# Optimization experiments

Hardware: AMD Instinct MI355X
Metric: run time of the kernel (lower is better)

## Reference

```python
import jax, jax.numpy as jnp
import numpy as np

B, T, R, E, H = 64, 512, 256, 512, 1024

def setup_inputs() -> dict:
    key = jax.random.key(0)
    ks = jax.random.split(key, 7)
    s = lambda d: 1.0 / np.sqrt(d)
    return {
        "x": jax.random.normal(ks[0], (B, T, R), jnp.float32),
        "W_emb": jax.random.normal(ks[1], (E, R), jnp.float32) * s(R),
        "b_emb": jax.random.normal(ks[2], (E,), jnp.float32) * s(R),
        "W_ih": jax.random.normal(ks[3], (4 * H, E), jnp.float32) * s(H),
        "W_hh": jax.random.normal(ks[4], (4 * H, H), jnp.float32) * s(H),
        "b_ih": jax.random.normal(ks[5], (4 * H,), jnp.float32) * s(H),
        "b_hh": jax.random.normal(ks[6], (4 * H,), jnp.float32) * s(H),
    }

def reference(x, W_emb, b_emb, W_ih, W_hh, b_ih, b_hh):
    # Per-timestep Linear embedding, batched over time (same math as the loop)
    xe = jnp.einsum('btr,er->bte', x, W_emb) + b_emb            # [B,T,E]
    # Input contribution to all gates, precomputed for every step
    gx = jnp.einsum('bte,ge->btg', xe, W_ih) + (b_ih + b_hh)    # [B,T,4H]

    def step(carry, gx_t):
        h, c = carry
        gates = gx_t + h @ W_hh.T                               # [B,4H]
        i, f, g, o = jnp.split(gates, 4, axis=-1)
        i = jax.nn.sigmoid(i)
        f = jax.nn.sigmoid(f)
        g = jnp.tanh(g)
        o = jax.nn.sigmoid(o)
        c_new = f * c + i * g
        h_new = o * jnp.tanh(c_new)
        return (h_new, c_new), h_new

    h0 = jnp.zeros((x.shape[0], H), x.dtype)
    c0 = jnp.zeros((x.shape[0], H), x.dtype)
    (h_t, c_t), ys = jax.lax.scan(step, (h0, c0), jnp.swapaxes(gx, 0, 1))
    outputs = jnp.swapaxes(ys, 0, 1)                            # [B,T,H]
    return outputs, h_t, c_t
```

## Files before the change

### kernel.cpp

```cpp
#include <hip/hip_runtime.h>
#include <stdint.h>

typedef __attribute__((ext_vector_type(8))) short short8;
typedef __attribute__((ext_vector_type(4))) float f32x4;
typedef __attribute__((ext_vector_type(4))) unsigned short ushort4v;
typedef unsigned long long u64;

__device__ inline unsigned short f2bf(float x) {
  union { float f; unsigned u; } v; v.f = x;
  unsigned r = (v.u + 0x7FFFu + ((v.u >> 16) & 1u)) >> 16;
  return (unsigned short)r;
}
__device__ inline float bf2f(unsigned short b) {
  union { unsigned u; float f; } v; v.u = ((unsigned)b) << 16;
  return v.f;
}
__device__ inline float fsig(float x) { return 1.f / (1.f + __expf(-x)); }

__device__ inline void gload_lds16(const void* g, void* l) {
  __builtin_amdgcn_global_load_lds(
      (const __attribute__((address_space(1))) unsigned int*)g,
      (__attribute__((address_space(3))) unsigned int*)l, 16, 0, 0);
}

__global__ void k_convert(const float* __restrict__ src, unsigned short* __restrict__ dst, int n4) {
  int i = blockIdx.x * blockDim.x + threadIdx.x;
  if (i < n4) {
    f32x4 v = *(const f32x4*)(src + (size_t)i * 4);
    ushort4v r;
    r.x = f2bf(v.x); r.y = f2bf(v.y); r.z = f2bf(v.z); r.w = f2bf(v.w);
    *(ushort4v*)(dst + (size_t)i * 4) = r;
  }
}

__global__ void k_bias(const float* __restrict__ a, const float* __restrict__ b,
                       float* __restrict__ o, int n) {
  int i = blockIdx.x * blockDim.x + threadIdx.x;
  if (i < n) o[i] = a[i] + b[i];
}

__global__ void k_init(unsigned short* __restrict__ h0, unsigned short* __restrict__ flags) {
  int i = blockIdx.x * blockDim.x + threadIdx.x;
  h0[i] = 0;
  if (i < 256) flags[i] = 0;
}

template <int MODE>
__global__ __launch_bounds__(256) void k_gemm_bt(
    const unsigned short* __restrict__ A,
    const unsigned short* __restrict__ Bm,
    const float* __restrict__ bias,
    unsigned short* __restrict__ C,
    int M, int N, int K) {
  __shared__ unsigned short As[128 * 32];
  __shared__ unsigned short Bs[128 * 32];
  const int tid = threadIdx.x;
  const int m0 = blockIdx.y * 128, n0 = blockIdx.x * 128;
  const int lane = tid & 63, w = tid >> 6;
  const int wm = (w >> 1) * 64, wn = (w & 1) * 64;

  f32x4 acc[4][4] = {};

  const int ar0 = tid >> 2;
  const int ak = (tid & 3) * 8;
  const unsigned short* Ag0 = A + (size_t)(m0 + ar0) * K + ak;
  const unsigned short* Ag1 = A + (size_t)(m0 + 64 + ar0) * K + ak;
  const unsigned short* Bg0 = Bm + (size_t)(n0 + ar0) * K + ak;
  const unsigned short* Bg1 = Bm + (size_t)(n0 + 64 + ar0) * K + ak;
  unsigned short* Al = As + tid * 8;
  unsigned short* Bl = Bs + tid * 8;

  const int lr = lane & 15, lk = (lane >> 4) * 8;

  for (int k0 = 0; k0 < K; k0 += 32) {
    gload_lds16(Ag0 + k0, Al);
    gload_lds16(Ag1 + k0, Al + 2048);
    gload_lds16(Bg0 + k0, Bl);
    gload_lds16(Bg1 + k0, Bl + 2048);
    __syncthreads();
    short8 a[4], b[4];
#pragma unroll
    for (int i = 0; i < 4; i++) a[i] = *(const short8*)&As[(wm + i * 16 + lr) * 32 + lk];
#pragma unroll
    for (int j = 0; j < 4; j++) b[j] = *(const short8*)&Bs[(wn + j * 16 + lr) * 32 + lk];
#pragma unroll
    for (int i = 0; i < 4; i++)
#pragma unroll
      for (int j = 0; j < 4; j++)
        acc[i][j] = __builtin_amdgcn_mfma_f32_16x16x32_bf16(a[i], b[j], acc[i][j], 0, 0, 0);
    __syncthreads();
  }

  const int lq = (lane >> 4) * 4;
#pragma unroll
  for (int j = 0; j < 4; j++) {
    int col = n0 + wn + j * 16 + lr;
    float bv = bias[col];
#pragma unroll
    for (int i = 0; i < 4; i++) {
      int rowb = m0 + wm + i * 16 + lq;
#pragma unroll
      for (int r = 0; r < 4; r++) {
        int row = rowb + r;
        float v = acc[i][j][r] + bv;
        if (MODE == 1) {
          int t = row & 511, bglob = row >> 9;
          int gg = bglob >> 4, bb = bglob & 15;
          int s = col >> 10, cc = col & 1023;
          int gtb = cc >> 4, cl = cc & 15;
          int wv = cl >> 2, qq = cl & 3;
          size_t idx = (size_t)t * 262144 + (size_t)gg * 65536 + (size_t)gtb * 1024
                     + (size_t)((wv * 64 + bb * 4 + qq) * 4 + s);
          C[idx] = f2bf(v);
        } else {
          C[(size_t)row * (size_t)N + col] = f2bf(v);
        }
      }
    }
  }
}

#define R32(F) F(0) F(1) F(2) F(3) F(4) F(5) F(6) F(7) \
               F(8) F(9) F(10) F(11) F(12) F(13) F(14) F(15) \
               F(16) F(17) F(18) F(19) F(20) F(21) F(22) F(23) \
               F(24) F(25) F(26) F(27) F(28) F(29) F(30) F(31)
#define WDECL(i) short8 w##i;
#define WLOAD(i) asm volatile("global_load_dwordx4 %0, %1, off offset:%c2" \
                              : "=v"(w##i) : "v"(wbase), "i"((i) * 64));
#define MFH(i, ACC) { \
    short8 a_ = *(const short8*)(HsB + ((lrB + (i) * 64) ^ sw)); \
    ACC = __builtin_amdgcn_mfma_f32_16x16x32_bf16(a_, w##i, ACC, 0, 0, 0); }
#define MF2(i, ACC) { \
    union { u64 d[2]; short8 s; } u_; \
    u_.d[0] = __hip_atomic_load((const u64*)(hrow2 + (i) * 32), __ATOMIC_RELAXED, __HIP_MEMORY_SCOPE_AGENT); \
    u_.d[1] = __hip_atomic_load((const u64*)(hrow2 + (i) * 32 + 4), __ATOMIC_RELAXED, __HIP_MEMORY_SCOPE_AGENT); \
    ACC = __builtin_amdgcn_mfma_f32_16x16x32_bf16(u_.s, w##i, ACC, 0, 0, 0); }

template <int RING>
__global__ __launch_bounds__(256, 1) void k_persist(
    const unsigned short* __restrict__ gx3,
    const unsigned short* __restrict__ Whh,
    unsigned short* __restrict__ hring,
    unsigned short* __restrict__ flags,
    float* __restrict__ out,
    float* __restrict__ hout,
    float* __restrict__ cout) {
  __shared__ unsigned short Hs[16384];
  __shared__ float Gs[4][16 * 17 + 4];

  const int tid = threadIdx.x;
  const int g = blockIdx.x & 3, gt = blockIdx.x >> 2;
  const int lane = tid & 63, w = tid >> 6;
  const int lr = lane & 15, hi = lane >> 4;

  const int grow = (lr >> 2) * 1024 + gt * 16 + w * 4 + (lr & 3);
  const unsigned short* wbase = Whh + (size_t)grow * 1024 + hi * 8;
  R32(WDECL)
  R32(WLOAD)
  asm volatile("s_waitcnt vmcnt(0)" ::: "memory");
  __builtin_amdgcn_sched_barrier(0);

  const int cb = lane >> 2, cq = lane & 3;
  const int col = gt * 16 + w * 4 + cq;
  const int brow = g * 16 + cb;
  float c_reg = 0.f;

  const u64* gbase = (const u64*)gx3 + (size_t)g * 16384 + (size_t)gt * 256;
  u64 gv = gbase[tid];

  const char* HsB = (const char*)Hs;
  const int lrB = lr * 2048 + hi * 16;
  const int sw = (lr & 7) << 4;

  for (int t = 0; t < 512; ++t) {
    if (w == 0) {
      const u64* fp = (const u64*)flags + g * 16 + lane;
      for (;;) {
        bool ok = true;
        if (lane < 16) {
          u64 f = __hip_atomic_load(fp, __ATOMIC_RELAXED, __HIP_MEMORY_SCOPE_AGENT);
          ok = ((int)(f & 0xFFFF) >= t) && ((int)((f >> 16) & 0xFFFF) >= t) &&
               ((int)((f >> 32) & 0xFFFF) >= t) && ((int)(f >> 48) >= t);
        }
        if (__all(ok)) break;
      }
    }
    __syncthreads();
    __builtin_amdgcn_sched_barrier(0);

    f32x4 ac0 = {}, ac1 = {}, ac2 = {}, ac3 = {};
    if (RING == 2) {
      const unsigned short* hrow2 = hring + (size_t)(t & 1) * 65536
                                  + (size_t)(g * 16 + lr) * 1024 + hi * 8;
      MF2(0, ac0)  MF2(1, ac1)  MF2(2, ac2)  MF2(3, ac3)
      MF2(4, ac0)  MF2(5, ac1)  MF2(6, ac2)  MF2(7, ac3)
      MF2(8, ac0)  MF2(9, ac1)  MF2(10, ac2) MF2(11, ac3)
      MF2(12, ac0) MF2(13, ac1) MF2(14, ac2) MF2(15, ac3)
      MF2(16, ac0) MF2(17, ac1) MF2(18, ac2) MF2(19, ac3)
      MF2(20, ac0) MF2(21, ac1) MF2(22, ac2) MF2(23, ac3)
      MF2(24, ac0) MF2(25, ac1) MF2(26, ac2) MF2(27, ac3)
      MF2(28, ac0) MF2(29, ac1) MF2(30, ac2) MF2(31, ac3)
    } else {
      const unsigned short* hsrc = hring + (size_t)t * 65536 + (size_t)g * 16384;
#pragma unroll
      for (int i = 0; i < 8; ++i) {
        int ch = w * 512 + i * 64;
        gload_lds16(hsrc + ((size_t)ch + lane) * 8, Hs + (size_t)ch * 8);
      }
      asm volatile("s_waitcnt vmcnt(0)" ::: "memory");
      __builtin_amdgcn_sched_barrier(0);
      __syncthreads();
      MFH(0, ac0)  MFH(1, ac1)  MFH(2, ac2)  MFH(3, ac3)
      MFH(4, ac0)  MFH(5, ac1)  MFH(6, ac2)  MFH(7, ac3)
      MFH(8, ac0)  MFH(9, ac1)  MFH(10, ac2) MFH(11, ac3)
      MFH(12, ac0) MFH(13, ac1) MFH(14, ac2) MFH(15, ac3)
      MFH(16, ac0) MFH(17, ac1) MFH(18, ac2) MFH(19, ac3)
      MFH(20, ac0) MFH(21, ac1) MFH(22, ac2) MFH(23, ac3)
      MFH(24, ac0) MFH(25, ac1) MFH(26, ac2) MFH(27, ac3)
      MFH(28, ac0) MFH(29, ac1) MFH(30, ac2) MFH(31, ac3)
    }
    f32x4 accs = (ac0 + ac1) + (ac2 + ac3);

#pragma unroll
    for (int r = 0; r < 4; ++r)
      Gs[w][(hi * 4 + r) * 17 + lr] = accs[r];
    asm volatile("s_waitcnt lgkmcnt(0)" ::: "memory");
    __builtin_amdgcn_sched_barrier(0);

    float gi = Gs[w][cb * 17 + 0 + cq]  + bf2f((unsigned short)(gv));
    float gf = Gs[w][cb * 17 + 4 + cq]  + bf2f((unsigned short)(gv >> 16));
    float gg = Gs[w][cb * 17 + 8 + cq]  + bf2f((unsigned short)(gv >> 32));
    float go = Gs[w][cb * 17 + 12 + cq] + bf2f((unsigned short)(gv >> 48));
    float i_ = fsig(gi);
    float f_ = fsig(gf);
    float g_ = tanhf(gg);
    float o_ = fsig(go);
    float cn = f_ * c_reg + i_ * g_;
    float hn = o_ * tanhf(cn);
    c_reg = cn;

    if (t == 511) {
      __builtin_nontemporal_store(hn, &out[((size_t)brow * 512 + t) * 1024 + col]);
      hout[(size_t)brow * 1024 + col] = hn;
      cout[(size_t)brow * 1024 + col] = cn;
    } else {
      unsigned hu = f2bf(hn);
      unsigned v0 = __shfl(hu, (lane & ~3) + 0);
      unsigned v1 = __shfl(hu, (lane & ~3) + 1);
      unsigned v2 = __shfl(hu, (lane & ~3) + 2);
      unsigned v3 = __shfl(hu, (lane & ~3) + 3);
      if ((lane & 3) == 0) {
        u64 pack = (u64)(v0 & 0xFFFF) | ((u64)(v1 & 0xFFFF) << 16)
                 | ((u64)(v2 & 0xFFFF) << 32) | ((u64)(v3 & 0xFFFF) << 48);
        u64* hp;
        if (RING == 2) {
          hp = (u64*)(hring + (size_t)((t + 1) & 1) * 65536
                      + (size_t)brow * 1024 + gt * 16 + w * 4);
        } else {
          size_t o = (size_t)brow * 2048 + (size_t)(gt * 16 + w * 4) * 2;
          o ^= (size_t)((brow & 7) << 4);
          hp = (u64*)((char*)hring + (size_t)(t + 1) * 131072 + o);
        }
        __hip_atomic_store(hp, pack, __ATOMIC_RELAXED, __HIP_MEMORY_SCOPE_AGENT);
      }
      __threadfence_block();
      __syncthreads();
      if (tid == 0)
        __hip_atomic_store(&flags[g * 64 + gt], (unsigned short)(t + 1),
                           __ATOMIC_RELAXED, __HIP_MEMORY_SCOPE_AGENT);
      __builtin_nontemporal_store(hn, &out[((size_t)brow * 512 + t) * 1024 + col]);
      gv = gbase[(size_t)(t + 1) * 65536 + tid];
    }
  }
}
#undef MF2
#undef MFH
#undef WLOAD
#undef WDECL
#undef R32

extern "C" void kernel_launch(void* const* d_in, const int* in_sizes, int n_in,
                              void* d_out, int out_size, void* d_ws, size_t ws_size,
                              hipStream_t stream) {
  const float* x = (const float*)d_in[0];
  const float* W_emb = (const float*)d_in[1];
  const float* b_emb = (const float*)d_in[2];
  const float* W_ih = (const float*)d_in[3];
  const float* W_hh = (const float*)d_in[4];
  const float* b_ih = (const float*)d_in[5];
  const float* b_hh = (const float*)d_in[6];

  char* ws = (char*)d_ws;
  unsigned short* x_bf    = (unsigned short*)(ws + 0);
  unsigned short* Wemb_bf = (unsigned short*)(ws + 16777216);
  unsigned short* Wih_bf  = (unsigned short*)(ws + 17039360);
  unsigned short* Whh_bf  = (unsigned short*)(ws + 21233664);
  float* bias_sum         = (float*)(ws + 29622272);
  unsigned short* xe      = (unsigned short*)(ws + 29638656);
  unsigned short* gx3     = (unsigned short*)(ws + 63193088);
  unsigned short* flags   = (unsigned short*)(ws + 331628544);
  unsigned short* hring   = (unsigned short*)(ws + 331632640);

  const size_t need_ring = 331632640ull + 512ull * 131072ull;
  const bool big = (ws_size >= need_ring);

  float* out = (float*)d_out;
  float* hout = out + (size_t)64 * 512 * 1024;
  float* cout = hout + 65536;

  k_convert<<<8192, 256, 0, stream>>>(x, x_bf, 2097152);
  k_convert<<<128, 256, 0, stream>>>(W_emb, Wemb_bf, 32768);
  k_convert<<<2048, 256, 0, stream>>>(W_ih, Wih_bf, 524288);
  k_convert<<<4096, 256, 0, stream>>>(W_hh, Whh_bf, 1048576);
  k_bias<<<16, 256, 0, stream>>>(b_ih, b_hh, bias_sum, 4096);
  k_init<<<256, 256, 0, stream>>>(hring, flags);

  k_gemm_bt<0><<<dim3(4, 256), 256, 0, stream>>>(x_bf, Wemb_bf, b_emb, xe, 32768, 512, 256);
  k_gemm_bt<1><<<dim3(32, 256), 256, 0, stream>>>(xe, Wih_bf, bias_sum, gx3, 32768, 4096, 512);

  if (big)
    k_persist<512><<<256, 256, 0, stream>>>(gx3, Whh_bf, hring, flags, out, hout, cout);
  else
    k_persist<2><<<256, 256, 0, stream>>>(gx3, Whh_bf, hring, flags, out, hout, cout);
}
```

Before: 2.163 ms.

## Use per-wave completion flags and transpose h staging into LDS on load

Each wave now publishes its own step flag after waiting for its h store, so the block-wide barrier before signalling is gone. Consumers poll 64 flags per group using all lanes instead of 16 packed ones. The h ring drops the XOR-swizzled layout and stays row-major, and the global-to-LDS copy gathers rows so that LDS ends up in the MFMA-friendly order without a swizzle. This is meant to cut synchronisation latency on the serial critical path, at the cost of more flag polling traffic and strided global gathers.

```diff
diff --git a/kernel.cpp b/kernel.cpp
--- a/kernel.cpp
+++ b/kernel.cpp
@@ -42,7 +42,7 @@
 __global__ void k_init(unsigned short* __restrict__ h0, unsigned short* __restrict__ flags) {
   int i = blockIdx.x * blockDim.x + threadIdx.x;
   h0[i] = 0;
-  if (i < 256) flags[i] = 0;
+  if (i < 1024) flags[i] = 0;
 }
 
 template <int MODE>
@@ -128,7 +128,7 @@
 #define WLOAD(i) asm volatile("global_load_dwordx4 %0, %1, off offset:%c2" \
                               : "=v"(w##i) : "v"(wbase), "i"((i) * 64));
 #define MFH(i, ACC) { \
-    short8 a_ = *(const short8*)(HsB + ((lrB + (i) * 64) ^ sw)); \
+    short8 a_ = *(const short8*)(HsB + lB + (i) * 1024); \
     ACC = __builtin_amdgcn_mfma_f32_16x16x32_bf16(a_, w##i, ACC, 0, 0, 0); }
 #define MF2(i, ACC) { \
     union { u64 d[2]; short8 s; } u_; \
@@ -169,19 +169,15 @@
   u64 gv = gbase[tid];
 
   const char* HsB = (const char*)Hs;
-  const int lrB = lr * 2048 + hi * 16;
-  const int sw = (lr & 7) << 4;
+  const int lB = hi * 256 + lr * 16;
 
   for (int t = 0; t < 512; ++t) {
     if (w == 0) {
-      const u64* fp = (const u64*)flags + g * 16 + lane;
+      const u64* fp = (const u64*)(flags + (size_t)g * 256) + lane;
       for (;;) {
-        bool ok = true;
-        if (lane < 16) {
-          u64 f = __hip_atomic_load(fp, __ATOMIC_RELAXED, __HIP_MEMORY_SCOPE_AGENT);
-          ok = ((int)(f & 0xFFFF) >= t) && ((int)((f >> 16) & 0xFFFF) >= t) &&
-               ((int)((f >> 32) & 0xFFFF) >= t) && ((int)(f >> 48) >= t);
-        }
+        u64 f = __hip_atomic_load(fp, __ATOMIC_RELAXED, __HIP_MEMORY_SCOPE_AGENT);
+        bool ok = ((int)(f & 0xFFFF) >= t) && ((int)((f >> 16) & 0xFFFF) >= t) &&
+                  ((int)((f >> 32) & 0xFFFF) >= t) && ((int)(f >> 48) >= t);
         if (__all(ok)) break;
       }
     }
@@ -204,8 +200,10 @@
       const unsigned short* hsrc = hring + (size_t)t * 65536 + (size_t)g * 16384;
 #pragma unroll
       for (int i = 0; i < 8; ++i) {
-        int ch = w * 512 + i * 64;
-        gload_lds16(hsrc + ((size_t)ch + lane) * 8, Hs + (size_t)ch * 8);
+        int cbase = w * 512 + i * 64;
+        int c = cbase + lane;
+        gload_lds16(hsrc + (size_t)((c & 15) * 1024 + (c >> 4) * 8),
+                    Hs + (size_t)cbase * 8);
       }
       asm volatile("s_waitcnt vmcnt(0)" ::: "memory");
       __builtin_amdgcn_sched_barrier(0);
@@ -252,21 +250,15 @@
       if ((lane & 3) == 0) {
         u64 pack = (u64)(v0 & 0xFFFF) | ((u64)(v1 & 0xFFFF) << 16)
                  | ((u64)(v2 & 0xFFFF) << 32) | ((u64)(v3 & 0xFFFF) << 48);
-        u64* hp;
-        if (RING == 2) {
-          hp = (u64*)(hring + (size_t)((t + 1) & 1) * 65536
-                      + (size_t)brow * 1024 + gt * 16 + w * 4);
-        } else {
-          size_t o = (size_t)brow * 2048 + (size_t)(gt * 16 + w * 4) * 2;
-          o ^= (size_t)((brow & 7) << 4);
-          hp = (u64*)((char*)hring + (size_t)(t + 1) * 131072 + o);
-        }
+        int wslot = (RING == 2) ? ((t + 1) & 1) : (t + 1);
+        u64* hp = (u64*)(hring + (size_t)wslot * 65536
+                         + (size_t)brow * 1024 + gt * 16 + w * 4);
         __hip_atomic_store(hp, pack, __ATOMIC_RELAXED, __HIP_MEMORY_SCOPE_AGENT);
       }
-      __threadfence_block();
-      __syncthreads();
-      if (tid == 0)
-        __hip_atomic_store(&flags[g * 64 + gt], (unsigned short)(t + 1),
+      asm volatile("s_waitcnt vmcnt(0)" ::: "memory");
+      __builtin_amdgcn_sched_barrier(0);
+      if (lane == 0)
+        __hip_atomic_store(&flags[(size_t)g * 256 + gt * 4 + w], (unsigned short)(t + 1),
                            __ATOMIC_RELAXED, __HIP_MEMORY_SCOPE_AGENT);
       __builtin_nontemporal_store(hn, &out[((size_t)brow * 512 + t) * 1024 + col]);
       gv = gbase[(size_t)(t + 1) * 65536 + tid];
```

New measurement: 3.086 ms. 42.7% more time.
